# Performance work log

Hardware: AMD Instinct MI355X
Metric: run time of the kernel (lower is better)

The kernel has to match this reference:

```python
import jax, jax.numpy as jnp
import numpy as np

N_NODE = 4095
D_EMB = 32
D_MODEL = 64
NHEADS = 8
ALPHA = 1.0
B = N_NODE + 1  # batch must equal n_node+1 (see einsum 'nm,tmd->tnd')
T = 32


def setup_inputs() -> dict:
    key = jax.random.key(0)
    ks = jax.random.split(key, 16)
    f32 = jnp.float32
    inp = {
        "q": jax.random.normal(ks[0], (B, T, D_MODEL), f32),
        "k": jax.random.normal(ks[1], (B, T, D_MODEL), f32),
        "v": jax.random.normal(ks[2], (B, T, D_MODEL), f32),
        # learned parameters (torch init is randn; scaled for numeric stability)
        "emb": jax.random.normal(ks[3], (N_NODE + 1, D_EMB), f32) * 0.05,
        "We": jax.random.normal(ks[4], (D_EMB, D_MODEL, D_MODEL), f32) * 0.05,
        "be": jax.random.normal(ks[5], (D_EMB, D_MODEL), f32) * 0.05,
        "Wq": jax.random.normal(ks[6], (D_MODEL, D_MODEL), f32) * 0.05,
        "bq": jax.random.normal(ks[7], (D_MODEL,), f32) * 0.05,
        "Wk": jax.random.normal(ks[8], (D_MODEL, D_MODEL), f32) * 0.05,
        "bk": jax.random.normal(ks[9], (D_MODEL,), f32) * 0.05,
        "Wv": jax.random.normal(ks[10], (D_MODEL, D_MODEL), f32) * 0.05,
        "bv": jax.random.normal(ks[11], (D_MODEL,), f32) * 0.05,
        "Wo": jax.random.normal(ks[12], (D_MODEL, D_MODEL), f32) * 0.05,
        "bo": jax.random.normal(ks[13], (D_MODEL,), f32) * 0.05,
    }
    return inp


def _elu(x, alpha):
    return jnp.where(x > 0, x, alpha * (jnp.exp(x) - 1.0))


def _split_heads(x, h):
    # torch.cat(torch.split(x, D//h, dim=-1), dim=0): [B,T,D] -> [h*B,T,D/h]
    b, t, d = x.shape
    return jnp.moveaxis(x.reshape(b, t, h, d // h), 2, 0).reshape(h * b, t, d // h)


def _merge_heads(x, b, h):
    # torch.cat(torch.split(x, B, dim=0), dim=-1): [h*B,T,D/h] -> [B,T,D]
    hb, t, dh = x.shape
    return jnp.moveaxis(x.reshape(h, b, t, dh), 0, 2).reshape(b, t, h * dh)


def reference(q, k, v, emb, We, be, Wq, bq, Wk, bk, Wv, bv, Wo, bo):
    Bq, Tq, D = q.shape
    h = NHEADS
    scale = (D // h) ** 0.5

    # linear projections (torch Linear: x @ W.T + b)
    q = q @ Wq.T + bq
    k = k @ Wk.T + bk
    v = v @ Wv.T + bv

    # adjacency: sum over d_emb of pairwise diff == s_i - s_j (same math, no [N,N,E] tensor)
    s = jnp.sum(emb, axis=-1)  # [N+1]
    sim = s[:, None] - s[None, :]  # [N+1, N+1]
    A = jax.nn.softmax(_elu(sim, ALPHA), axis=-1) + jnp.eye(Bq, dtype=q.dtype)

    # updateQ: adjacency-weighted diffusion + per-node weight matrices
    qt = jnp.transpose(q, (1, 0, 2))  # [T, N, D]
    W = jnp.einsum('ne,eio->nio', emb, We)  # [N, D, D]
    b = emb @ be  # [N, D]
    q_ = jnp.einsum('nm,tmd->tnd', A, qt)  # diffusion
    q_ = jnp.einsum('tnd,ndo->tno', q_, W) + b  # per-node matmul
    q = jnp.transpose(q_, (1, 0, 2))  # [N, T, D]

    # manual multi-head attention via split/cat
    qh = _split_heads(q, h)
    kh = _split_heads(k, h)
    vh = _split_heads(v, h)
    attn = jax.nn.softmax(jnp.einsum('btd,bsd->bts', qh, kh) / scale, axis=-1)
    out = jnp.einsum('bts,bsd->btd', attn, vh)
    out = _merge_heads(out, Bq, h)
    return out @ Wo.T + bo
```

## Files before the change

kernel.cpp:

```cpp
#include <hip/hip_runtime.h>
#include <hip/hip_bf16.h>

constexpr int NN  = 4096;
constexpr int DE  = 32;
constexpr int TD  = 2048;

typedef __attribute__((ext_vector_type(8))) short short8;
typedef __attribute__((ext_vector_type(4))) float f32x4;

#define MFMA16(a, b, c) __builtin_amdgcn_mfma_f32_16x16x32_bf16(a, b, c, 0, 0, 0)

__device__ inline ushort f2b(float x) {
    __hip_bfloat16 h = __float2bfloat16(x);
    union { __hip_bfloat16 h; ushort u; } c; c.h = h;
    return c.u;
}

__device__ inline float b2f(ushort u) {
    union { unsigned u; float f; } c; c.u = ((unsigned)u) << 16;
    return c.f;
}

__device__ inline short8 pack8(float4 a, float4 b) {
    short8 v;
    v[0] = (short)f2b(a.x); v[1] = (short)f2b(a.y); v[2] = (short)f2b(a.z); v[3] = (short)f2b(a.w);
    v[4] = (short)f2b(b.x); v[5] = (short)f2b(b.y); v[6] = (short)f2b(b.z); v[7] = (short)f2b(b.w);
    return v;
}

__device__ inline short8 pack8v(f32x4 a, f32x4 b) {
    short8 v;
    v[0] = (short)f2b(a[0]); v[1] = (short)f2b(a[1]); v[2] = (short)f2b(a[2]); v[3] = (short)f2b(a[3]);
    v[4] = (short)f2b(b[0]); v[5] = (short)f2b(b[1]); v[6] = (short)f2b(b[2]); v[7] = (short)f2b(b[3]);
    return v;
}

__device__ __forceinline__ short8 as_s8(f32x4 v) {
    union { f32x4 f; short8 s; } u; u.f = v; return u.s;
}

template<int OFF>
__device__ __forceinline__ f32x4 gl16(unsigned long long addr) {
    f32x4 d;
    asm volatile("global_load_dwordx4 %0, %1, off offset:%c2"
                 : "=v"(d) : "v"(addr), "n"(OFF) : "memory");
    return d;
}

template<int OFF>
__device__ __forceinline__ float gl4(unsigned long long addr) {
    float d;
    asm volatile("global_load_dword %0, %1, off offset:%c2"
                 : "=v"(d) : "v"(addr), "n"(OFF) : "memory");
    return d;
}

#define WAITV(N) asm volatile("s_waitcnt vmcnt(" #N ")" ::: "memory"); \
                 __builtin_amdgcn_sched_barrier(0)

__global__ __launch_bounds__(256) void k_prep(const float* __restrict__ emb,
                                              const float* __restrict__ We,
                                              const float* __restrict__ be,
                                              const float* __restrict__ Wk,
                                              const float* __restrict__ Wv,
                                              const float* __restrict__ Wo,
                                              float* __restrict__ s_g,
                                              ushort* __restrict__ embbf,
                                              ushort* __restrict__ WeTT,
                                              ushort* __restrict__ Wkbf,
                                              ushort* __restrict__ Wvbf,
                                              ushort* __restrict__ Wobf,
                                              float* __restrict__ bn) {
    int id = blockIdx.x, tid = threadIdx.x;
    if (id < 16) {
        int n = id * 256 + tid;
        const float4* e4 = (const float4*)(emb + n * DE);
        float s = 0.f;
#pragma unroll
        for (int i = 0; i < DE / 4; ++i) { float4 v = e4[i]; s += v.x + v.y + v.z + v.w; }
        s_g[n] = s;
    } else if (id < 144) {
        int g4 = (id - 16) * 256 + tid;
        float4 v = *(const float4*)&emb[(size_t)g4 * 4];
        ushort4 o; o.x = f2b(v.x); o.y = f2b(v.y); o.z = f2b(v.z); o.w = f2b(v.w);
        *(ushort4*)&embbf[(size_t)g4 * 4] = o;
    } else if (id < 176) {
        int e = id - 144;
#pragma unroll
        for (int u = 0; u < 4; ++u) {
            int idx0 = tid * 16 + u * 4;
            float4 v = *(const float4*)&We[(size_t)e * 4096 + idx0];
            float vv[4] = {v.x, v.y, v.z, v.w};
#pragma unroll
            for (int i = 0; i < 4; ++i) {
                int idx = idx0 + i;
                int o = idx & 63, d = idx >> 6;
                WeTT[(size_t)(o * 64 + d) * 32 + e] = f2b(vv[i]);
            }
        }
    } else if (id < 224) {
        int id5 = id - 176;
        int which = id5 >> 4, gid = (id5 & 15) * 256 + tid;
        const float* src = which == 0 ? Wk : (which == 1 ? Wv : Wo);
        ushort* dst = which == 0 ? Wkbf : (which == 1 ? Wvbf : Wobf);
        dst[gid] = f2b(src[gid]);
    } else {
        int gid = (id - 224) * 256 + tid;
        int n = gid >> 6, o = gid & 63;
        float acc = 0.f;
#pragma unroll
        for (int e = 0; e < DE; ++e) acc += emb[n * DE + e] * be[e * 64 + o];
        bn[gid] = acc;
    }
}

__global__ __launch_bounds__(256) void k_pr(const float* __restrict__ X,
                                            const float* __restrict__ W,
                                            const float* __restrict__ bias,
                                            ushort* __restrict__ Y,
                                            const float* __restrict__ s_g,
                                            int* __restrict__ perm) {
    __shared__ float ss[NN];
    int id = blockIdx.x, tid = threadIdx.x;
    if (id < 512) {
        int lane = tid & 63, wid = tid >> 6;
        int r0 = id * 256 + wid * 64;
        int l15 = lane & 15, kb = lane >> 4;
        f32x4 acc[4][4] = {};
#pragma unroll
        for (int kk = 0; kk < 2; ++kk) {
            short8 af[4], bf[4];
#pragma unroll
            for (int f = 0; f < 4; ++f) {
                const float* ap = X + (size_t)(r0 + f * 16 + l15) * 64 + kk * 32 + kb * 8;
                af[f] = pack8(*(const float4*)ap, *(const float4*)(ap + 4));
                const float* bp = W + (size_t)(f * 16 + l15) * 64 + kk * 32 + kb * 8;
                bf[f] = pack8(*(const float4*)bp, *(const float4*)(bp + 4));
            }
#pragma unroll
            for (int i = 0; i < 4; ++i)
#pragma unroll
                for (int j = 0; j < 4; ++j)
                    acc[i][j] = MFMA16(af[i], bf[j], acc[i][j]);
        }
        float bcol[4];
#pragma unroll
        for (int j = 0; j < 4; ++j) bcol[j] = bias[j * 16 + l15];
#pragma unroll
        for (int i = 0; i < 4; ++i)
#pragma unroll
            for (int j = 0; j < 4; ++j)
#pragma unroll
                for (int r = 0; r < 4; ++r)
                    Y[(size_t)(r0 + i * 16 + kb * 4 + r) * 64 + j * 16 + l15] =
                        f2b(acc[i][j][r] + bcol[j]);
    } else {
        for (int i = tid; i < NN; i += 256) ss[i] = s_g[i];
        __syncthreads();
        int g = tid >> 5, l = tid & 31;
        int n = (id - 512) * 8 + g;
        float sn = ss[n];
        int cnt = 0;
        for (int j2 = 0; j2 < 128; ++j2) {
            int m = j2 * 32 + l;
            float sm = ss[m];
            cnt += (sm < sn) || (sm == sn && m < n);
        }
        for (int off = 16; off; off >>= 1) cnt += __shfl_down(cnt, off, 32);
        if (l == 0) perm[cnt] = n;
    }
}

__global__ __launch_bounds__(256) void k_csum(const ushort* __restrict__ qp,
                                              const float* __restrict__ s_g,
                                              const int* __restrict__ perm,
                                              float* __restrict__ Cj,
                                              float* __restrict__ Cb) {
    __shared__ int ns[64];
    __shared__ float bs[64];
    int bx = blockIdx.x, by = blockIdx.y, tid = threadIdx.x;
    if (tid < 64) {
        int n = perm[bx * 64 + tid];
        ns[tid] = n;
        bs[tid] = __expf(-s_g[n]);
    }
    __syncthreads();
    int j = by * 256 + tid;
    float run[8] = {};
    for (int ii = 0; ii < 64; ++ii) {
        float qv = b2f(qp[(size_t)ns[ii] * 2048 + j]);
        float b = bs[ii], t = qv;
#pragma unroll
        for (int k2 = 0; k2 < 8; ++k2) { run[k2] += t; t *= b; }
    }
    float* cp = Cj + ((size_t)bx * 2048 + j) * 8;
    *(float4*)cp       = make_float4(run[0], run[1], run[2], run[3]);
    *(float4*)(cp + 4) = make_float4(run[4], run[5], run[6], run[7]);
    if (by == 0 && tid < 64) {
        float b = bs[tid], bk = 1.f;
#pragma unroll
        for (int k2 = 0; k2 < 8; ++k2) {
            float v = bk;
            for (int off = 32; off; off >>= 1) v += __shfl_down(v, off, 64);
            if (tid == 0) Cb[bx * 8 + k2] = v;
            bk *= b;
        }
    }
}

__global__ __launch_bounds__(256) void k_pre(const float* __restrict__ Cj,
                                             float* __restrict__ PRE,
                                             const float* __restrict__ Cb,
                                             float* __restrict__ CbPre) {
    __shared__ float sCb[512];
    int tid = threadIdx.x;
    if (blockIdx.x < 64) {
        int gid = blockIdx.x * 256 + tid;
        float run = 0.f;
#pragma unroll 8
        for (int c = 0; c < 64; ++c) {
            PRE[(size_t)c * 16384 + gid] = run;
            run += Cj[(size_t)c * 16384 + gid];
        }
        PRE[(size_t)64 * 16384 + gid] = run;
    } else {
        sCb[tid] = Cb[tid];
        sCb[tid + 256] = Cb[tid + 256];
        __syncthreads();
        if (tid < 8) {
            float run = 0.f;
            for (int c = 0; c < 64; ++c) {
                CbPre[c * 8 + tid] = run;
                run += sCb[c * 8 + tid];
            }
            CbPre[512 + tid] = run;
        }
    }
}

__global__ __launch_bounds__(256) void k_combw(const ushort* __restrict__ qp,
                                               const float* __restrict__ s_g,
                                               const int* __restrict__ perm,
                                               const float* __restrict__ PRE,
                                               const float* __restrict__ CbPre,
                                               ushort* __restrict__ qdifb,
                                               const ushort* __restrict__ embbf,
                                               const ushort* __restrict__ WeTT,
                                               ushort* __restrict__ WnT) {
    __shared__ int ns[64];
    __shared__ float sa[64], sb[64];
    int id = blockIdx.x, tid = threadIdx.x;
    if (id < 512) {
        int bx = id & 63, by = id >> 6;
        if (tid < 64) {
            int n = perm[bx * 64 + tid];
            ns[tid] = n;
            float s = s_g[n];
            sa[tid] = __expf(s);
            sb[tid] = __expf(-s);
        }
        __syncthreads();
        int j = by * 256 + tid;
        float T[8], pre[8];
        {
            const float* pp = PRE + (size_t)bx * 16384 + (size_t)j * 8;
            float4 u0 = *(const float4*)pp, u1 = *(const float4*)(pp + 4);
            pre[0] = u0.x; pre[1] = u0.y; pre[2] = u0.z; pre[3] = u0.w;
            pre[4] = u1.x; pre[5] = u1.y; pre[6] = u1.z; pre[7] = u1.w;
            const float* tp = PRE + (size_t)64 * 16384 + (size_t)j * 8;
            float4 t0 = *(const float4*)tp, t1 = *(const float4*)(tp + 4);
            T[0] = t0.x; T[1] = t0.y; T[2] = t0.z; T[3] = t0.w;
            T[4] = t1.x; T[5] = t1.y; T[6] = t1.z; T[7] = t1.w;
        }
        float TB[8], preb[8];
        {
            float4 v0 = *(const float4*)&CbPre[bx * 8], v1 = *(const float4*)&CbPre[bx * 8 + 4];
            preb[0] = v0.x; preb[1] = v0.y; preb[2] = v0.z; preb[3] = v0.w;
            preb[4] = v1.x; preb[5] = v1.y; preb[6] = v1.z; preb[7] = v1.w;
            float4 t0 = *(const float4*)&CbPre[512], t1 = *(const float4*)&CbPre[516];
            TB[0] = t0.x; TB[1] = t0.y; TB[2] = t0.z; TB[3] = t0.w;
            TB[4] = t1.x; TB[5] = t1.y; TB[6] = t1.z; TB[7] = t1.w;
        }
#pragma unroll 2
        for (int ii = 0; ii < 64; ++ii) {
            int n = ns[ii];
            float a = sa[ii], b = sb[ii];
            float g0 = 0.36787944117144233f;
            float g1 = g0 * a;
            float g2 = g1 * a * 0.5f;
            float g3 = g2 * a * (1.f / 3.f);
            float g4 = g3 * a * 0.25f;
            float g5 = g4 * a * 0.2f;
            float g6 = g5 * a * (1.f / 6.f);
            float g7 = g6 * a * (1.f / 7.f);
            float Z = a * preb[1]
                    + g0 * (TB[0] - preb[0]) + g1 * (TB[1] - preb[1])
                    + g2 * (TB[2] - preb[2]) + g3 * (TB[3] - preb[3])
                    + g4 * (TB[4] - preb[4]) + g5 * (TB[5] - preb[5])
                    + g6 * (TB[6] - preb[6]) + g7 * (TB[7] - preb[7]);
            float izv = 1.f / Z;
            float qv = b2f(qp[(size_t)n * 2048 + j]);
            float ss2 = g0 * (T[0] - pre[0]) + g1 * (T[1] - pre[1])
                      + g2 * (T[2] - pre[2]) + g3 * (T[3] - pre[3])
                      + g4 * (T[4] - pre[4]) + g5 * (T[5] - pre[5])
                      + g6 * (T[6] - pre[6]) + g7 * (T[7] - pre[7]);
            float outv = (a * pre[1] + ss2) * izv + qv;
            qdifb[(size_t)n * 2048 + j] = f2b(outv);
            float bk = 1.f;
#pragma unroll
            for (int k2 = 0; k2 < 8; ++k2) { pre[k2] += bk * qv; preb[k2] += bk; bk *= b; }
        }
    } else {
        int w2 = id - 512;
        int lane = tid & 63, wid = tid >> 6;
        int n0  = (w2 & 31) * 128 + (wid >> 1) * 64;
        int od0 = (w2 >> 5) * 128 + (wid & 1) * 64;
        int l15 = lane & 15, kb = lane >> 4;
        short8 af[4], bf[4];
#pragma unroll
        for (int f = 0; f < 4; ++f) {
            af[f] = *(const short8*)(embbf + (size_t)(n0 + f * 16 + l15) * 32 + kb * 8);
            bf[f] = *(const short8*)(WeTT + (size_t)(od0 + f * 16 + l15) * 32 + kb * 8);
        }
        f32x4 acc[4][4] = {};
#pragma unroll
        for (int i = 0; i < 4; ++i)
#pragma unroll
            for (int j = 0; j < 4; ++j)
                acc[i][j] = MFMA16(af[i], bf[j], acc[i][j]);
#pragma unroll
        for (int i = 0; i < 4; ++i)
#pragma unroll
            for (int j = 0; j < 4; ++j)
#pragma unroll
                for (int r = 0; r < 4; ++r)
                    WnT[(size_t)(n0 + i * 16 + kb * 4 + r) * 4096 + od0 + j * 16 + l15] =
                        f2b(acc[i][j][r]);
    }
}

__global__ __launch_bounds__(128, 2) void k_fused(const float* __restrict__ kin,
                                                  const float* __restrict__ vin,
                                                  const ushort* __restrict__ qdifb,
                                                  const ushort* __restrict__ WnT,
                                                  const float* __restrict__ bn,
                                                  const ushort* __restrict__ Wkbf,
                                                  const float* __restrict__ bk,
                                                  const ushort* __restrict__ Wvbf,
                                                  const float* __restrict__ bv,
                                                  const ushort* __restrict__ Wobf,
                                                  const float* __restrict__ bo,
                                                  float* __restrict__ out) {
    __shared__ ushort Kb[2176];
    __shared__ ushort Qb[2176];
    __shared__ ushort Vb[2560];
    __shared__ ushort Pb[2][1280];
    __shared__ ushort attb[2304];
    int tid = threadIdx.x, lane = tid & 63, w = tid >> 6;
    int b = blockIdx.x;
    int l15 = lane & 15, g = lane >> 4;
    int hh_w = l15 >> 3, d1_w = l15 & 7;
    const float SCALE = 0.35355339059327373f;
    short8 zfrag = {};

    const float*  xin = w ? vin : kin;
    const ushort* Wx  = w ? Wvbf : Wkbf;
    const float*  bx_ = w ? bv : bk;

    unsigned long long bxA = (unsigned long long)(bx_ + l15);
    unsigned long long bnA = (unsigned long long)(bn + (size_t)b * 64 + w * 32 + l15);
    unsigned long long boA = (unsigned long long)(bo + w * 32 + l15);
    unsigned long long wxA = (unsigned long long)((const char*)Wx + l15 * 128 + g * 16 + 3072);
    unsigned long long xaA = (unsigned long long)(xin + (size_t)b * TD + (8 + l15) * 64 + g * 8);
    unsigned long long qaA = (unsigned long long)(qdifb + (size_t)b * TD + (8 + l15) * 64 + g * 8);
    unsigned long long wnA = (unsigned long long)((const char*)(WnT + (size_t)b * 4096) + w * 4096 + l15 * 128 + g * 16 + 1024);
    unsigned long long woA = (unsigned long long)((const char*)Wobf + w * 4096 + l15 * 128 + g * 16 + 1024);

    float bxc[4], bnc[2], boc[2];
    bxc[0] = gl4<0>(bxA); bxc[1] = gl4<64>(bxA); bxc[2] = gl4<128>(bxA); bxc[3] = gl4<192>(bxA);
    bnc[0] = gl4<0>(bnA); bnc[1] = gl4<64>(bnA);
    boc[0] = gl4<0>(boA); boc[1] = gl4<64>(boA);
    f32x4 wx00 = gl16<-3072>(wxA), wx01 = gl16<-3008>(wxA);
    f32x4 wx10 = gl16<-1024>(wxA), wx11 = gl16< -960>(wxA);
    f32x4 wx20 = gl16< 1024>(wxA), wx21 = gl16< 1088>(wxA);
    f32x4 wx30 = gl16< 3072>(wxA), wx31 = gl16< 3136>(wxA);
    f32x4 x00a = gl16<-2048>(xaA), x00b = gl16<-2032>(xaA);
    f32x4 x01a = gl16<-1920>(xaA), x01b = gl16<-1904>(xaA);
    f32x4 x10a = gl16< 2048>(xaA), x10b = gl16< 2064>(xaA);
    f32x4 x11a = gl16< 2176>(xaA), x11b = gl16< 2192>(xaA);
    f32x4 q00 = gl16<-1024>(qaA), q01 = gl16<-960>(qaA);
    f32x4 q10 = gl16< 1024>(qaA), q11 = gl16<1088>(qaA);
    f32x4 wn00 = gl16<-1024>(wnA), wn01 = gl16<-960>(wnA);
    f32x4 wn10 = gl16< 1024>(wnA), wn11 = gl16<1088>(wnA);
    f32x4 wo00 = gl16<-1024>(woA), wo01 = gl16<-960>(woA);
    f32x4 wo10 = gl16< 1024>(woA), wo11 = gl16<1088>(woA);

    WAITV(12);
    {
        short8 xaf[2][2], wxf[4][2];
        xaf[0][0] = pack8v(x00a, x00b); xaf[1][0] = pack8v(x01a, x01b);
        xaf[0][1] = pack8v(x10a, x10b); xaf[1][1] = pack8v(x11a, x11b);
        wxf[0][0] = as_s8(wx00); wxf[0][1] = as_s8(wx01);
        wxf[1][0] = as_s8(wx10); wxf[1][1] = as_s8(wx11);
        wxf[2][0] = as_s8(wx20); wxf[2][1] = as_s8(wx21);
        wxf[3][0] = as_s8(wx30); wxf[3][1] = as_s8(wx31);
#pragma unroll
        for (int j = 0; j < 4; ++j) {
            f32x4 ax[2] = {};
#pragma unroll
            for (int kk = 0; kk < 2; ++kk)
#pragma unroll
                for (int ti = 0; ti < 2; ++ti)
                    ax[ti] = MFMA16(xaf[kk][ti], wxf[j][kk], ax[ti]);
            if (w == 0) {
#pragma unroll
                for (int ti = 0; ti < 2; ++ti)
#pragma unroll
                    for (int r = 0; r < 4; ++r) {
                        int s = ti * 16 + g * 4 + r;
                        Kb[(j * 2 + hh_w) * 272 + s * 8 + d1_w] = f2b(ax[ti][r] + bxc[j]);
                    }
            } else {
#pragma unroll
                for (int ti = 0; ti < 2; ++ti)
#pragma unroll
                    for (int r = 0; r < 4; r += 2) {
                        int s = ti * 16 + g * 4 + r;
                        ushort2 p; p.x = f2b(ax[ti][r] + bxc[j]); p.y = f2b(ax[ti][r + 1] + bxc[j]);
                        *(ushort2*)&Vb[(j * 2 + hh_w) * 320 + d1_w * 40 + s] = p;
                    }
            }
        }
    }

    WAITV(4);
    {
        short8 qaf[2][2], wnf[2][2];
        qaf[0][0] = as_s8(q00); qaf[1][0] = as_s8(q01);
        qaf[0][1] = as_s8(q10); qaf[1][1] = as_s8(q11);
        wnf[0][0] = as_s8(wn00); wnf[0][1] = as_s8(wn01);
        wnf[1][0] = as_s8(wn10); wnf[1][1] = as_s8(wn11);
#pragma unroll
        for (int jj = 0; jj < 2; ++jj) {
            int j = 2 * w + jj;
            f32x4 aq[2] = {};
#pragma unroll
            for (int kk = 0; kk < 2; ++kk)
#pragma unroll
                for (int ti = 0; ti < 2; ++ti)
                    aq[ti] = MFMA16(qaf[kk][ti], wnf[jj][kk], aq[ti]);
#pragma unroll
            for (int ti = 0; ti < 2; ++ti)
#pragma unroll
                for (int r = 0; r < 4; ++r) {
                    int s = ti * 16 + g * 4 + r;
                    Qb[(j * 2 + hh_w) * 272 + s * 8 + d1_w] = f2b(aq[ti][r] + bnc[jj]);
                }
        }
    }
    __syncthreads();

#pragma unroll
    for (int hh = 0; hh < 4; ++hh) {
        int h = 4 * w + hh;
        short8 kf[2], qf[2];
#pragma unroll
        for (int si = 0; si < 2; ++si)
            kf[si] = (lane < 16) ? *(const short8*)&Kb[h * 272 + (si * 16 + l15) * 8] : zfrag;
#pragma unroll
        for (int ti = 0; ti < 2; ++ti)
            qf[ti] = (lane < 16) ? *(const short8*)&Qb[h * 272 + (ti * 16 + l15) * 8] : zfrag;
        f32x4 sc[2][2];
#pragma unroll
        for (int si = 0; si < 2; ++si)
#pragma unroll
            for (int ti = 0; ti < 2; ++ti)
                sc[si][ti] = MFMA16(kf[si], qf[ti], f32x4{});
#pragma unroll
        for (int ti = 0; ti < 2; ++ti) {
            float e0[4], e1[4], sm = 0.f;
#pragma unroll
            for (int r = 0; r < 4; ++r) {
                e0[r] = __expf(sc[0][ti][r] * SCALE);
                e1[r] = __expf(sc[1][ti][r] * SCALE);
                sm += e0[r] + e1[r];
            }
            sm += __shfl_xor(sm, 16);
            sm += __shfl_xor(sm, 32);
            float inv = 1.f / sm;
            int t = ti * 16 + l15;
            unsigned p00 = (unsigned)f2b(e0[0] * inv) | ((unsigned)f2b(e0[1] * inv) << 16);
            unsigned p01 = (unsigned)f2b(e0[2] * inv) | ((unsigned)f2b(e0[3] * inv) << 16);
            unsigned p10 = (unsigned)f2b(e1[0] * inv) | ((unsigned)f2b(e1[1] * inv) << 16);
            unsigned p11 = (unsigned)f2b(e1[2] * inv) | ((unsigned)f2b(e1[3] * inv) << 16);
            *(unsigned*)&Pb[w][t * 40 + g * 4]          = p00;
            *(unsigned*)&Pb[w][t * 40 + g * 4 + 2]      = p01;
            *(unsigned*)&Pb[w][t * 40 + 16 + g * 4]     = p10;
            *(unsigned*)&Pb[w][t * 40 + 16 + g * 4 + 2] = p11;
        }
        short8 vf = *(const short8*)&Vb[h * 320 + (l15 & 7) * 40 + g * 8];
#pragma unroll
        for (int ti = 0; ti < 2; ++ti) {
            short8 af = *(const short8*)&Pb[w][(ti * 16 + l15) * 40 + g * 8];
            f32x4 pv = MFMA16(af, vf, f32x4{});
            if (l15 < 8) {
#pragma unroll
                for (int r = 0; r < 4; ++r)
                    attb[(ti * 16 + g * 4 + r) * 72 + h * 8 + l15] = f2b(pv[r]);
            }
        }
    }
    __syncthreads();

    WAITV(0);
    {
        short8 wof[2][2];
        wof[0][0] = as_s8(wo00); wof[0][1] = as_s8(wo01);
        wof[1][0] = as_s8(wo10); wof[1][1] = as_s8(wo11);
        short8 aof[2][2];
#pragma unroll
        for (int kk = 0; kk < 2; ++kk)
#pragma unroll
            for (int ti = 0; ti < 2; ++ti)
                aof[kk][ti] = *(const short8*)&attb[(ti * 16 + l15) * 72 + kk * 32 + g * 8];
#pragma unroll
        for (int jj = 0; jj < 2; ++jj) {
            int j = 2 * w + jj;
            f32x4 co[2] = {};
#pragma unroll
            for (int kk = 0; kk < 2; ++kk)
#pragma unroll
                for (int ti = 0; ti < 2; ++ti)
                    co[ti] = MFMA16(aof[kk][ti], wof[jj][kk], co[ti]);
#pragma unroll
            for (int ti = 0; ti < 2; ++ti)
#pragma unroll
                for (int r = 0; r < 4; ++r)
                    out[(size_t)b * TD + (ti * 16 + g * 4 + r) * 64 + j * 16 + l15] =
                        co[ti][r] + boc[jj];
        }
    }
}

extern "C" void kernel_launch(void* const* d_in, const int* in_sizes, int n_in,
                              void* d_out, int out_size, void* d_ws, size_t ws_size,
                              hipStream_t stream) {
    const float* q   = (const float*)d_in[0];
    const float* k   = (const float*)d_in[1];
    const float* v   = (const float*)d_in[2];
    const float* emb = (const float*)d_in[3];
    const float* We  = (const float*)d_in[4];
    const float* be  = (const float*)d_in[5];
    const float* Wq  = (const float*)d_in[6];
    const float* bq  = (const float*)d_in[7];
    const float* Wk  = (const float*)d_in[8];
    const float* bk  = (const float*)d_in[9];
    const float* Wv  = (const float*)d_in[10];
    const float* bv  = (const float*)d_in[11];
    const float* Wo  = (const float*)d_in[12];
    const float* bo  = (const float*)d_in[13];

    float* ws = (float*)d_ws;
    ushort* qp    = (ushort*)ws;
    ushort* WnT   = (ushort*)(ws + 4194304);
    ushort* qdifb = (ushort*)(ws + 12582912);
    float*  Cj    = ws + 16777216;
    float*  bn    = ws + 17825792;
    float*  s_g   = ws + 18087936;
    int*    perm  = (int*)(ws + 18092032);
    float*  Cb    = ws + 18096128;
    ushort* embbf = (ushort*)(ws + 18096640);
    ushort* WeTT  = (ushort*)(ws + 18162176);
    ushort* Wkbf  = (ushort*)(ws + 18227712);
    ushort* Wvbf  = (ushort*)(ws + 18229760);
    ushort* Wobf  = (ushort*)(ws + 18231808);
    float*  PRE   = ws + 18233856;
    float*  CbPre = ws + 19298816;
    float*  outp  = (float*)d_out;

    k_prep <<<1248, 256, 0, stream>>>(emb, We, be, Wk, Wv, Wo,
                                      s_g, embbf, WeTT, Wkbf, Wvbf, Wobf, bn);
    k_pr   <<<1024, 256, 0, stream>>>(q, Wq, bq, qp, s_g, perm);
    k_csum <<<dim3(64, 8), 256, 0, stream>>>(qp, s_g, perm, Cj, Cb);
    k_pre  <<<65, 256, 0, stream>>>(Cj, PRE, Cb, CbPre);
    k_combw<<<1536, 256, 0, stream>>>(qp, s_g, perm, PRE, CbPre, qdifb,
                                      embbf, WeTT, WnT);
    k_fused<<<4096, 128, 0, stream>>>(k, v, qdifb, WnT, bn,
                                      Wkbf, bk, Wvbf, bv, Wobf, bo, outp);
}
```

Measured before the change: 109.9 us.

## Split fused attention kernel work across four waves per block instead of two

```diff
diff --git a/kernel.cpp b/kernel.cpp
--- a/kernel.cpp
+++ b/kernel.cpp
@@ -339,7 +339,7 @@
     }
 }
 
-__global__ __launch_bounds__(128, 2) void k_fused(const float* __restrict__ kin,
+__global__ __launch_bounds__(256, 2) void k_fused(const float* __restrict__ kin,
                                                   const float* __restrict__ vin,
                                                   const ushort* __restrict__ qdifb,
                                                   const ushort* __restrict__ WnT,
@@ -354,7 +354,7 @@
     __shared__ ushort Kb[2176];
     __shared__ ushort Qb[2176];
     __shared__ ushort Vb[2560];
-    __shared__ ushort Pb[2][1280];
+    __shared__ ushort Pb[4][1280];
     __shared__ ushort attb[2304];
     int tid = threadIdx.x, lane = tid & 63, w = tid >> 6;
     int b = blockIdx.x;
@@ -363,47 +363,60 @@
     const float SCALE = 0.35355339059327373f;
     short8 zfrag = {};
 
-    const float*  xin = w ? vin : kin;
-    const ushort* Wx  = w ? Wvbf : Wkbf;
-    const float*  bx_ = w ? bv : bk;
-
-    unsigned long long bxA = (unsigned long long)(bx_ + l15);
-    unsigned long long bnA = (unsigned long long)(bn + (size_t)b * 64 + w * 32 + l15);
-    unsigned long long boA = (unsigned long long)(bo + w * 32 + l15);
-    unsigned long long wxA = (unsigned long long)((const char*)Wx + l15 * 128 + g * 16 + 3072);
-    unsigned long long xaA = (unsigned long long)(xin + (size_t)b * TD + (8 + l15) * 64 + g * 8);
-    unsigned long long qaA = (unsigned long long)(qdifb + (size_t)b * TD + (8 + l15) * 64 + g * 8);
-    unsigned long long wnA = (unsigned long long)((const char*)(WnT + (size_t)b * 4096) + w * 4096 + l15 * 128 + g * 16 + 1024);
-    unsigned long long woA = (unsigned long long)((const char*)Wobf + w * 4096 + l15 * 128 + g * 16 + 1024);
-
-    float bxc[4], bnc[2], boc[2];
-    bxc[0] = gl4<0>(bxA); bxc[1] = gl4<64>(bxA); bxc[2] = gl4<128>(bxA); bxc[3] = gl4<192>(bxA);
-    bnc[0] = gl4<0>(bnA); bnc[1] = gl4<64>(bnA);
-    boc[0] = gl4<0>(boA); boc[1] = gl4<64>(boA);
-    f32x4 wx00 = gl16<-3072>(wxA), wx01 = gl16<-3008>(wxA);
-    f32x4 wx10 = gl16<-1024>(wxA), wx11 = gl16< -960>(wxA);
-    f32x4 wx20 = gl16< 1024>(wxA), wx21 = gl16< 1088>(wxA);
-    f32x4 wx30 = gl16< 3072>(wxA), wx31 = gl16< 3136>(wxA);
-    f32x4 x00a = gl16<-2048>(xaA), x00b = gl16<-2032>(xaA);
-    f32x4 x01a = gl16<-1920>(xaA), x01b = gl16<-1904>(xaA);
-    f32x4 x10a = gl16< 2048>(xaA), x10b = gl16< 2064>(xaA);
-    f32x4 x11a = gl16< 2176>(xaA), x11b = gl16< 2192>(xaA);
-    f32x4 q00 = gl16<-1024>(qaA), q01 = gl16<-960>(qaA);
-    f32x4 q10 = gl16< 1024>(qaA), q11 = gl16<1088>(qaA);
-    f32x4 wn00 = gl16<-1024>(wnA), wn01 = gl16<-960>(wnA);
-    f32x4 wn10 = gl16< 1024>(wnA), wn11 = gl16<1088>(wnA);
-    f32x4 wo00 = gl16<-1024>(woA), wo01 = gl16<-960>(woA);
-    f32x4 wo10 = gl16< 1024>(woA), wo11 = gl16<1088>(woA);
-
-    WAITV(12);
+    f32x4 wx0, wx1, wx2, wx3, wx4, wx5, wx6, wx7;
+    f32x4 x0, x1, x2, x3, x4, x5, x6, x7;
+    float bxc0, bxc1, bxc2, bxc3;
+    f32x4 q0v, q1v, q2v, q3v;
+    f32x4 wn0, wn1, wn2, wn3;
+    float bnc0, bnc1;
+    f32x4 wo0, wo1; float boc;
+
+    if (w < 2) {
+        const float*  xin = w ? vin : kin;
+        const ushort* Wx  = w ? Wvbf : Wkbf;
+        const float*  bx_ = w ? bv : bk;
+        unsigned long long bxA = (unsigned long long)(bx_ + l15);
+        unsigned long long wxA = (unsigned long long)((const char*)Wx + l15 * 128 + g * 16 + 3072);
+        unsigned long long xaA = (unsigned long long)(xin + (size_t)b * TD + (8 + l15) * 64 + g * 8);
+        bxc0 = gl4<0>(bxA); bxc1 = gl4<64>(bxA); bxc2 = gl4<128>(bxA); bxc3 = gl4<192>(bxA);
+        wx0 = gl16<-3072>(wxA); wx1 = gl16<-3008>(wxA);
+        wx2 = gl16<-1024>(wxA); wx3 = gl16< -960>(wxA);
+        wx4 = gl16< 1024>(wxA); wx5 = gl16< 1088>(wxA);
+        wx6 = gl16< 3072>(wxA); wx7 = gl16< 3136>(wxA);
+        x0 = gl16<-2048>(xaA); x1 = gl16<-2032>(xaA);
+        x2 = gl16<-1920>(xaA); x3 = gl16<-1904>(xaA);
+        x4 = gl16< 2048>(xaA); x5 = gl16< 2064>(xaA);
+        x6 = gl16< 2176>(xaA); x7 = gl16< 2192>(xaA);
+    } else {
+        int wq = w - 2;
+        unsigned long long qaA = (unsigned long long)(qdifb + (size_t)b * TD + (8 + l15) * 64 + g * 8);
+        unsigned long long wnA = (unsigned long long)((const char*)(WnT + (size_t)b * 4096)
+                                                      + ((size_t)(wq * 32 + l15)) * 128 + g * 16);
+        unsigned long long bnA = (unsigned long long)(bn + (size_t)b * 64 + wq * 32 + l15);
+        q0v = gl16<-1024>(qaA); q1v = gl16<-960>(qaA);
+        q2v = gl16< 1024>(qaA); q3v = gl16<1088>(qaA);
+        wn0 = gl16<0>(wnA); wn1 = gl16<64>(wnA);
+        wn2 = gl16<2048>(wnA); wn3 = gl16<2112>(wnA);
+        bnc0 = gl4<0>(bnA); bnc1 = gl4<64>(bnA);
+    }
     {
+        unsigned long long woA = (unsigned long long)((const char*)Wobf
+                                                      + ((size_t)(w * 16 + l15)) * 128 + g * 16);
+        unsigned long long boA = (unsigned long long)(bo + w * 16 + l15);
+        wo0 = gl16<0>(woA); wo1 = gl16<64>(woA);
+        boc = gl4<0>(boA);
+    }
+
+    if (w < 2) {
+        WAITV(3);
         short8 xaf[2][2], wxf[4][2];
-        xaf[0][0] = pack8v(x00a, x00b); xaf[1][0] = pack8v(x01a, x01b);
-        xaf[0][1] = pack8v(x10a, x10b); xaf[1][1] = pack8v(x11a, x11b);
-        wxf[0][0] = as_s8(wx00); wxf[0][1] = as_s8(wx01);
-        wxf[1][0] = as_s8(wx10); wxf[1][1] = as_s8(wx11);
-        wxf[2][0] = as_s8(wx20); wxf[2][1] = as_s8(wx21);
-        wxf[3][0] = as_s8(wx30); wxf[3][1] = as_s8(wx31);
+        xaf[0][0] = pack8v(x0, x1); xaf[1][0] = pack8v(x2, x3);
+        xaf[0][1] = pack8v(x4, x5); xaf[1][1] = pack8v(x6, x7);
+        wxf[0][0] = as_s8(wx0); wxf[0][1] = as_s8(wx1);
+        wxf[1][0] = as_s8(wx2); wxf[1][1] = as_s8(wx3);
+        wxf[2][0] = as_s8(wx4); wxf[2][1] = as_s8(wx5);
+        wxf[3][0] = as_s8(wx6); wxf[3][1] = as_s8(wx7);
+        float bxc[4] = {bxc0, bxc1, bxc2, bxc3};
 #pragma unroll
         for (int j = 0; j < 4; ++j) {
             f32x4 ax[2] = {};
@@ -431,18 +444,18 @@
                     }
             }
         }
-    }
-
-    WAITV(4);
-    {
+    } else {
+        int wq = w - 2;
+        WAITV(3);
         short8 qaf[2][2], wnf[2][2];
-        qaf[0][0] = as_s8(q00); qaf[1][0] = as_s8(q01);
-        qaf[0][1] = as_s8(q10); qaf[1][1] = as_s8(q11);
-        wnf[0][0] = as_s8(wn00); wnf[0][1] = as_s8(wn01);
-        wnf[1][0] = as_s8(wn10); wnf[1][1] = as_s8(wn11);
+        qaf[0][0] = as_s8(q0v); qaf[1][0] = as_s8(q1v);
+        qaf[0][1] = as_s8(q2v); qaf[1][1] = as_s8(q3v);
+        wnf[0][0] = as_s8(wn0); wnf[0][1] = as_s8(wn1);
+        wnf[1][0] = as_s8(wn2); wnf[1][1] = as_s8(wn3);
+        float bnc[2] = {bnc0, bnc1};
 #pragma unroll
         for (int jj = 0; jj < 2; ++jj) {
-            int j = 2 * w + jj;
+            int j = 2 * wq + jj;
             f32x4 aq[2] = {};
 #pragma unroll
             for (int kk = 0; kk < 2; ++kk)
@@ -461,8 +474,8 @@
     __syncthreads();
 
 #pragma unroll
-    for (int hh = 0; hh < 4; ++hh) {
-        int h = 4 * w + hh;
+    for (int hh = 0; hh < 2; ++hh) {
+        int h = 2 * w + hh;
         short8 kf[2], qf[2];
 #pragma unroll
         for (int si = 0; si < 2; ++si)
@@ -514,31 +527,26 @@
 
     WAITV(0);
     {
-        short8 wof[2][2];
-        wof[0][0] = as_s8(wo00); wof[0][1] = as_s8(wo01);
-        wof[1][0] = as_s8(wo10); wof[1][1] = as_s8(wo11);
+        short8 wof[2];
+        wof[0] = as_s8(wo0); wof[1] = as_s8(wo1);
         short8 aof[2][2];
 #pragma unroll
         for (int kk = 0; kk < 2; ++kk)
 #pragma unroll
             for (int ti = 0; ti < 2; ++ti)
                 aof[kk][ti] = *(const short8*)&attb[(ti * 16 + l15) * 72 + kk * 32 + g * 8];
-#pragma unroll
-        for (int jj = 0; jj < 2; ++jj) {
-            int j = 2 * w + jj;
-            f32x4 co[2] = {};
-#pragma unroll
-            for (int kk = 0; kk < 2; ++kk)
-#pragma unroll
-                for (int ti = 0; ti < 2; ++ti)
-                    co[ti] = MFMA16(aof[kk][ti], wof[jj][kk], co[ti]);
+        f32x4 co[2] = {};
+#pragma unroll
+        for (int kk = 0; kk < 2; ++kk)
 #pragma unroll
             for (int ti = 0; ti < 2; ++ti)
-#pragma unroll
-                for (int r = 0; r < 4; ++r)
-                    out[(size_t)b * TD + (ti * 16 + g * 4 + r) * 64 + j * 16 + l15] =
-                        co[ti][r] + boc[jj];
-        }
+                co[ti] = MFMA16(aof[kk][ti], wof[kk], co[ti]);
+#pragma unroll
+        for (int ti = 0; ti < 2; ++ti)
+#pragma unroll
+            for (int r = 0; r < 4; ++r)
+                out[(size_t)b * TD + (ti * 16 + g * 4 + r) * 64 + w * 16 + l15] =
+                    co[ti][r] + boc;
     }
 }
 
@@ -585,6 +593,6 @@
     k_pre  <<<65, 256, 0, stream>>>(Cj, PRE, Cb, CbPre);
     k_combw<<<1536, 256, 0, stream>>>(qp, s_g, perm, PRE, CbPre, qdifb,
                                       embbf, WeTT, WnT);
-    k_fused<<<4096, 128, 0, stream>>>(k, v, qdifb, WnT, bn,
+    k_fused<<<4096, 256, 0, stream>>>(k, v, qdifb, WnT, bn,
                                       Wkbf, bk, Wvbf, bv, Wobf, bo, outp);
 }
```

New measurement: 107.0 us. 1.03x faster.
